# Kernel optimization log

Hardware: AMD Instinct MI355X
Metric: run time of the kernel (lower is better)

## Reference

```python
import jax, jax.numpy as jnp
import numpy as np

N, C, C_OUT, E = 50000, 128, 256, 600000


def setup_inputs() -> dict:
    key = jax.random.key(0)
    k1, k2, k3, k4, k5 = jax.random.split(key, 5)
    x = jax.random.normal(k1, (N, C), dtype=jnp.float32)
    edge_index = jax.random.randint(k2, (2, E), 0, N, dtype=jnp.int64)
    # torch Linear(2C -> C_OUT): weight [out, in], bias [out]
    bound = 1.0 / np.sqrt(2 * C)
    W = jax.random.uniform(k3, (C_OUT, 2 * C), dtype=jnp.float32, minval=-bound, maxval=bound)
    b = jax.random.uniform(k4, (C_OUT,), dtype=jnp.float32, minval=-bound, maxval=bound)
    return {"x": x, "edge_index": edge_index, "W": W, "b": b}


def reference(x, edge_index, W, b):
    src, dst = edge_index[0], edge_index[1]
    # gather - subtract: relative features per edge [E, C]
    rel = x[src] - x[dst]
    # scatter-max into destination nodes; empty segments -> 0 (torch_scatter fill)
    x_j = jax.ops.segment_max(rel, dst, num_segments=N)
    x_j = jnp.where(jnp.isfinite(x_j), x_j, 0.0)
    # concat + Linear + ReLU (MLP([2C, C_OUT], act='relu'))
    h = jnp.concatenate([x, x_j], axis=1)  # [N, 2C]
    out = h @ W.T + b
    return jax.nn.relu(out)
```

## Files before the change

### kernel.cpp

```cpp
#include <hip/hip_runtime.h>

#define NNODES 50000
#define CIN    128
#define COUT   256
#define KTOT   256

#define POISON 0xAAAAAAAAu

typedef float  f32x4  __attribute__((ext_vector_type(4)));
typedef short  bf16x8 __attribute__((ext_vector_type(8)));

#define GLOAD16(gptr, lptr) __builtin_amdgcn_global_load_lds(                      \
    (const __attribute__((address_space(1))) void*)(gptr),                         \
    (__attribute__((address_space(3))) void*)(lptr), 16, 0, 0)

__device__ __forceinline__ unsigned short f2bf(float f) {
    union { float f; unsigned int u; } v; v.f = f;
    unsigned int r = v.u + 0x7FFFu + ((v.u >> 16) & 1u);
    return (unsigned short)(r >> 16);
}
__device__ __forceinline__ float bf2f(unsigned short u) {
    return __uint_as_float((unsigned int)u << 16);
}

#define PX 1600000
#define PW (PX + 16384)

__global__ __launch_bounds__(256)
void prep_hist(const float* __restrict__ x, const float* __restrict__ W,
               const int* __restrict__ dst,
               unsigned short* __restrict__ xcat, unsigned short* __restrict__ Wbf,
               int* __restrict__ cnt, int E) {
    int g = blockIdx.x * 256 + threadIdx.x;
    if (g < PX) {
        float4 v = ((const float4*)x)[g];
        int row = g >> 5;
        int col = (g & 31) * 4;
        *(ushort4*)(xcat + (size_t)row * KTOT + col) =
            make_ushort4(f2bf(v.x), f2bf(v.y), f2bf(v.z), f2bf(v.w));
    } else if (g < PW) {
        int i = g - PX;
        float4 v = ((const float4*)W)[i];
        *(ushort4*)(Wbf + (size_t)i * 4) =
            make_ushort4(f2bf(v.x), f2bf(v.y), f2bf(v.z), f2bf(v.w));
    } else {
        int i = g - PW;
        if (i < E) atomicAdd(&cnt[dst[i]], 1);
    }
}

__global__ __launch_bounds__(256)
void scan_kernel(const int* __restrict__ cnt, int* __restrict__ row_start) {
    __shared__ int red[256];
    __shared__ int s[256];
    const int tid    = threadIdx.x;
    const int chunk0 = blockIdx.x * 256;

    int acc = 0;
    for (int i = tid; i < chunk0; i += 256)
        acc += (int)((unsigned)cnt[i] - POISON);
    red[tid] = acc;
    __syncthreads();
    for (int off = 128; off > 0; off >>= 1) {
        if (tid < off) red[tid] += red[tid + off];
        __syncthreads();
    }
    int base = red[0];

    int i = chunk0 + tid;
    int v = (i < NNODES) ? (int)((unsigned)cnt[i] - POISON) : 0;
    s[tid] = v;
    __syncthreads();
    for (int off = 1; off < 256; off <<= 1) {
        int t = (tid >= off) ? s[tid - off] : 0;
        __syncthreads();
        s[tid] += t;
        __syncthreads();
    }
    if (i < NNODES) row_start[i] = base + s[tid] - v;
    if (i == NNODES - 1) row_start[NNODES] = base + s[tid];
}

__global__ void scatter_kernel(const int* __restrict__ src, const int* __restrict__ dst,
                               const int* __restrict__ row_start, int* __restrict__ cnt,
                               int* __restrict__ sorted_src, int E) {
    int i = blockIdx.x * blockDim.x + threadIdx.x;
    if (i < E) {
        int d = dst[i];
        int old = atomicSub(&cnt[d], 1);
        int pos = (int)((unsigned)old - POISON) - 1;
        sorted_src[row_start[d] + pos] = src[i];
    }
}

__device__ __forceinline__ float2 fmax2(float2 a, float2 b) {
    return make_float2(fmaxf(a.x, b.x), fmaxf(a.y, b.y));
}

__global__ __launch_bounds__(256)
void gather_max_kernel(const float* __restrict__ x,
                       const int* __restrict__ row_start,
                       const int* __restrict__ sorted_src,
                       unsigned short* __restrict__ xcat) {
    int wid  = (blockIdx.x * blockDim.x + threadIdx.x) >> 6;
    int lane = threadIdx.x & 63;
    if (wid >= NNODES) return;

    int start = row_start[wid];
    int end   = row_start[wid + 1];

    const float NI = __int_as_float(0xFF800000u);
    float2 mm[8];
#pragma unroll
    for (int j = 0; j < 8; ++j) mm[j] = make_float2(NI, NI);

    int t = start;
    for (; t + 8 <= end; t += 8) {
        int     si[8];
        ushort2 uu[8];
#pragma unroll
        for (int j = 0; j < 8; ++j) si[j] = sorted_src[t + j];
#pragma unroll
        for (int j = 0; j < 8; ++j)
            uu[j] = *(const ushort2*)(xcat + (size_t)si[j] * KTOT + lane * 2);
#pragma unroll
        for (int j = 0; j < 8; ++j)
            mm[j] = fmax2(mm[j], make_float2(bf2f(uu[j].x), bf2f(uu[j].y)));
    }
    for (; t < end; ++t) {
        int s = sorted_src[t];
        ushort2 u = *(const ushort2*)(xcat + (size_t)s * KTOT + lane * 2);
        mm[0] = fmax2(mm[0], make_float2(bf2f(u.x), bf2f(u.y)));
    }
    float2 mx = fmax2(fmax2(fmax2(mm[0], mm[1]), fmax2(mm[2], mm[3])),
                      fmax2(fmax2(mm[4], mm[5]), fmax2(mm[6], mm[7])));

    float2 xv = ((const float2*)(x + (size_t)wid * CIN))[lane];
    bool nonempty = (end > start);
    float2 o;
    o.x = nonempty ? mx.x - xv.x : 0.0f;
    o.y = nonempty ? mx.y - xv.y : 0.0f;
    *((ushort2*)(xcat + (size_t)wid * KTOT + CIN + lane * 2)) =
        make_ushort2(f2bf(o.x), f2bf(o.y));
}

__global__ __launch_bounds__(256, 4)
void mfma_gemm(const unsigned short* __restrict__ xcat,
               const unsigned short* __restrict__ Wbf,
               const float* __restrict__ bias,
               float* __restrict__ out) {
    __shared__ unsigned short As[2][64][32];
    __shared__ unsigned short Bs[2][256][32];

    const int M = NNODES;
    const int m0 = blockIdx.x * 64;

    const int tid  = threadIdx.x;
    const int lane = tid & 63;
    const int wid  = tid >> 6;

    f32x4 acc[4][4] = {};

    auto stage = [&](int b, int kt) {
        {
            int row  = tid >> 2;
            int kseg = (tid & 3) * 8;
            int ks   = kseg ^ ((row & 3) << 3);
            int grow = m0 + row; if (grow > M - 1) grow = M - 1;
            GLOAD16(xcat + (size_t)grow * KTOT + kt + ks, &As[b][row][kseg]);
        }
#pragma unroll
        for (int j = 0; j < 4; ++j) {
            int u    = j * 256 + tid;
            int row  = u >> 2;
            int kseg = (u & 3) * 8;
            int ks   = kseg ^ ((row & 3) << 3);
            GLOAD16(Wbf + (size_t)row * KTOT + kt + ks, &Bs[b][row][kseg]);
        }
    };

    stage(0, 0);
    __syncthreads();

    const int l15 = lane & 15;
    const int kh  = (lane >> 4) * 8;
    const int khs = kh ^ ((l15 & 3) << 3);

#pragma unroll
    for (int t = 0; t < 8; ++t) {
        int b = t & 1;
        if (t < 7) stage(b ^ 1, (t + 1) * 32);

        bf16x8 af[4], bfr[4];
#pragma unroll
        for (int m = 0; m < 4; ++m)
            af[m] = *(const bf16x8*)&As[b][m * 16 + l15][khs];
#pragma unroll
        for (int n = 0; n < 4; ++n)
            bfr[n] = *(const bf16x8*)&Bs[b][wid * 64 + n * 16 + l15][khs];
#pragma unroll
        for (int m = 0; m < 4; ++m)
#pragma unroll
            for (int n = 0; n < 4; ++n)
                acc[m][n] = __builtin_amdgcn_mfma_f32_16x16x32_bf16(af[m], bfr[n], acc[m][n], 0, 0, 0);

        __syncthreads();
    }

#pragma unroll
    for (int n = 0; n < 4; ++n) {
        int col = wid * 64 + n * 16 + l15;
        float bv = bias[col];
#pragma unroll
        for (int m = 0; m < 4; ++m) {
            int r0 = m0 + m * 16 + ((lane >> 4) << 2);
            f32x4 a = acc[m][n];
#pragma unroll
            for (int r = 0; r < 4; ++r) {
                int rr = r0 + r;
                if (rr < M) out[(size_t)rr * COUT + col] = fmaxf(a[r] + bv, 0.0f);
            }
        }
    }
}

extern "C" void kernel_launch(void* const* d_in, const int* in_sizes, int n_in,
                              void* d_out, int out_size, void* d_ws, size_t ws_size,
                              hipStream_t stream) {
    const float* x  = (const float*)d_in[0];
    const int*   ei = (const int*)d_in[1];
    const float* W  = (const float*)d_in[2];
    const float* b  = (const float*)d_in[3];
    float*       out = (float*)d_out;

    const int E = in_sizes[1] / 2;
    const int* src = ei;
    const int* dst = ei + E;

    unsigned short* xcat       = (unsigned short*)d_ws;
    unsigned short* Wbf        = xcat + (size_t)NNODES * KTOT;
    int*            cnt        = (int*)(Wbf + COUT * KTOT);
    int*            row_start  = cnt + NNODES;
    int*            sorted_src = row_start + (NNODES + 1);

    const int NB_N = (NNODES + 255) / 256;
    const int NB_E = (E + 255) / 256;

    prep_hist<<<(PW + E + 255) / 256, 256, 0, stream>>>(x, W, dst, xcat, Wbf, cnt, E);
    scan_kernel<<<NB_N, 256, 0, stream>>>(cnt, row_start);
    scatter_kernel<<<NB_E, 256, 0, stream>>>(src, dst, row_start, cnt, sorted_src, E);
    gather_max_kernel<<<(NNODES * 64 + 255) / 256, 256, 0, stream>>>(x, row_start, sorted_src, xcat);
    mfma_gemm<<<(NNODES + 63) / 64, 256, 0, stream>>>(xcat, Wbf, b, out);
}
```

Measured before the change: 228.4 us.

## Fuse gather-max aggregation into the GEMM kernel via shared memory

Merges the per-node gather-max kernel into the MFMA GEMM. Each block computes the x_j half of its 64-row A tile directly into LDS, with swizzled columns, while the x half and the first W tile are loaded asynchronously. This removes one kernel launch and the global write and re-read of the x_j half of xcat. In exchange the GEMM block holds more LDS and runs at lower occupancy, and the irregular gather now runs with fewer waves, one node at a time per wave, before the MFMA loop starts.

```diff
diff --git a/kernel.cpp b/kernel.cpp
--- a/kernel.cpp
+++ b/kernel.cpp
@@ -97,78 +97,25 @@
     return make_float2(fmaxf(a.x, b.x), fmaxf(a.y, b.y));
 }
 
-__global__ __launch_bounds__(256)
-void gather_max_kernel(const float* __restrict__ x,
-                       const int* __restrict__ row_start,
-                       const int* __restrict__ sorted_src,
-                       unsigned short* __restrict__ xcat) {
-    int wid  = (blockIdx.x * blockDim.x + threadIdx.x) >> 6;
-    int lane = threadIdx.x & 63;
-    if (wid >= NNODES) return;
-
-    int start = row_start[wid];
-    int end   = row_start[wid + 1];
-
-    const float NI = __int_as_float(0xFF800000u);
-    float2 mm[8];
-#pragma unroll
-    for (int j = 0; j < 8; ++j) mm[j] = make_float2(NI, NI);
-
-    int t = start;
-    for (; t + 8 <= end; t += 8) {
-        int     si[8];
-        ushort2 uu[8];
-#pragma unroll
-        for (int j = 0; j < 8; ++j) si[j] = sorted_src[t + j];
-#pragma unroll
-        for (int j = 0; j < 8; ++j)
-            uu[j] = *(const ushort2*)(xcat + (size_t)si[j] * KTOT + lane * 2);
-#pragma unroll
-        for (int j = 0; j < 8; ++j)
-            mm[j] = fmax2(mm[j], make_float2(bf2f(uu[j].x), bf2f(uu[j].y)));
-    }
-    for (; t < end; ++t) {
-        int s = sorted_src[t];
-        ushort2 u = *(const ushort2*)(xcat + (size_t)s * KTOT + lane * 2);
-        mm[0] = fmax2(mm[0], make_float2(bf2f(u.x), bf2f(u.y)));
-    }
-    float2 mx = fmax2(fmax2(fmax2(mm[0], mm[1]), fmax2(mm[2], mm[3])),
-                      fmax2(fmax2(mm[4], mm[5]), fmax2(mm[6], mm[7])));
-
-    float2 xv = ((const float2*)(x + (size_t)wid * CIN))[lane];
-    bool nonempty = (end > start);
-    float2 o;
-    o.x = nonempty ? mx.x - xv.x : 0.0f;
-    o.y = nonempty ? mx.y - xv.y : 0.0f;
-    *((ushort2*)(xcat + (size_t)wid * KTOT + CIN + lane * 2)) =
-        make_ushort2(f2bf(o.x), f2bf(o.y));
-}
-
-__global__ __launch_bounds__(256, 4)
-void mfma_gemm(const unsigned short* __restrict__ xcat,
-               const unsigned short* __restrict__ Wbf,
-               const float* __restrict__ bias,
-               float* __restrict__ out) {
-    __shared__ unsigned short As[2][64][32];
+__global__ __launch_bounds__(256, 2)
+void mrconv_gemm(const float* __restrict__ x,
+                 const unsigned short* __restrict__ xcat,
+                 const unsigned short* __restrict__ Wbf,
+                 const int* __restrict__ row_start,
+                 const int* __restrict__ sorted_src,
+                 const float* __restrict__ bias,
+                 float* __restrict__ out) {
+    __shared__ unsigned short As [64][128];
+    __shared__ unsigned short Axj[64][128];
     __shared__ unsigned short Bs[2][256][32];
 
-    const int M = NNODES;
-    const int m0 = blockIdx.x * 64;
-
+    const int M    = NNODES;
+    const int m0   = blockIdx.x * 64;
     const int tid  = threadIdx.x;
     const int lane = tid & 63;
-    const int wid  = tid >> 6;
-
-    f32x4 acc[4][4] = {};
-
-    auto stage = [&](int b, int kt) {
-        {
-            int row  = tid >> 2;
-            int kseg = (tid & 3) * 8;
-            int ks   = kseg ^ ((row & 3) << 3);
-            int grow = m0 + row; if (grow > M - 1) grow = M - 1;
-            GLOAD16(xcat + (size_t)grow * KTOT + kt + ks, &As[b][row][kseg]);
-        }
+    const int wv   = tid >> 6;
+
+    auto stageB = [&](int b, int kt) {
 #pragma unroll
         for (int j = 0; j < 4; ++j) {
             int u    = j * 256 + tid;
@@ -179,25 +126,82 @@
         }
     };
 
-    stage(0, 0);
+#pragma unroll
+    for (int j = 0; j < 4; ++j) {
+        int u   = j * 256 + tid;
+        int row = u >> 4;
+        int g   = u & 15;
+        int gs  = (g & 8) | ((g & 7) ^ (row & 7));
+        int grow = m0 + row; if (grow > M - 1) grow = M - 1;
+        GLOAD16(xcat + (size_t)grow * KTOT + gs * 8, &As[row][g * 8]);
+    }
+    stageB(0, 0);
+
+    const float NI = __int_as_float(0xFF800000u);
+    for (int i = 0; i < 16; ++i) {
+        int r    = wv * 16 + i;
+        int node = m0 + r; if (node > M - 1) node = M - 1;
+        int start = row_start[node];
+        int end   = row_start[node + 1];
+
+        float2 mm[8];
+#pragma unroll
+        for (int j = 0; j < 8; ++j) mm[j] = make_float2(NI, NI);
+
+        int t = start;
+        for (; t + 8 <= end; t += 8) {
+            int     si[8];
+            ushort2 uu[8];
+#pragma unroll
+            for (int j = 0; j < 8; ++j) si[j] = sorted_src[t + j];
+#pragma unroll
+            for (int j = 0; j < 8; ++j)
+                uu[j] = *(const ushort2*)(xcat + (size_t)si[j] * KTOT + lane * 2);
+#pragma unroll
+            for (int j = 0; j < 8; ++j)
+                mm[j] = fmax2(mm[j], make_float2(bf2f(uu[j].x), bf2f(uu[j].y)));
+        }
+        for (; t < end; ++t) {
+            int s = sorted_src[t];
+            ushort2 u = *(const ushort2*)(xcat + (size_t)s * KTOT + lane * 2);
+            mm[0] = fmax2(mm[0], make_float2(bf2f(u.x), bf2f(u.y)));
+        }
+        float2 mx = fmax2(fmax2(fmax2(mm[0], mm[1]), fmax2(mm[2], mm[3])),
+                          fmax2(fmax2(mm[4], mm[5]), fmax2(mm[6], mm[7])));
+
+        float2 xv = ((const float2*)(x + (size_t)node * CIN))[lane];
+        bool nonempty = (end > start);
+        float2 o;
+        o.x = nonempty ? mx.x - xv.x : 0.0f;
+        o.y = nonempty ? mx.y - xv.y : 0.0f;
+        int c = (lane * 2) ^ ((i & 7) << 3);
+        *(ushort2*)&Axj[r][c] = make_ushort2(f2bf(o.x), f2bf(o.y));
+    }
+
     __syncthreads();
 
     const int l15 = lane & 15;
     const int kh  = (lane >> 4) * 8;
-    const int khs = kh ^ ((l15 & 3) << 3);
+    const int l7s = (l15 & 7) << 3;
+    const int khsB = kh ^ ((l15 & 3) << 3);
+
+    f32x4 acc[4][4] = {};
 
 #pragma unroll
     for (int t = 0; t < 8; ++t) {
         int b = t & 1;
-        if (t < 7) stage(b ^ 1, (t + 1) * 32);
+        if (t < 7) stageB(b ^ 1, (t + 1) * 32);
 
         bf16x8 af[4], bfr[4];
 #pragma unroll
-        for (int m = 0; m < 4; ++m)
-            af[m] = *(const bf16x8*)&As[b][m * 16 + l15][khs];
+        for (int m = 0; m < 4; ++m) {
+            int row = m * 16 + l15;
+            if (t < 4) af[m] = *(const bf16x8*)&As [row][(t * 32 + kh) ^ l7s];
+            else       af[m] = *(const bf16x8*)&Axj[row][((t - 4) * 32 + kh) ^ l7s];
+        }
 #pragma unroll
         for (int n = 0; n < 4; ++n)
-            bfr[n] = *(const bf16x8*)&Bs[b][wid * 64 + n * 16 + l15][khs];
+            bfr[n] = *(const bf16x8*)&Bs[b][wv * 64 + n * 16 + l15][khsB];
 #pragma unroll
         for (int m = 0; m < 4; ++m)
 #pragma unroll
@@ -209,7 +213,7 @@
 
 #pragma unroll
     for (int n = 0; n < 4; ++n) {
-        int col = wid * 64 + n * 16 + l15;
+        int col = wv * 64 + n * 16 + l15;
         float bv = bias[col];
 #pragma unroll
         for (int m = 0; m < 4; ++m) {
@@ -249,6 +253,5 @@
     prep_hist<<<(PW + E + 255) / 256, 256, 0, stream>>>(x, W, dst, xcat, Wbf, cnt, E);
     scan_kernel<<<NB_N, 256, 0, stream>>>(cnt, row_start);
     scatter_kernel<<<NB_E, 256, 0, stream>>>(src, dst, row_start, cnt, sorted_src, E);
-    gather_max_kernel<<<(NNODES * 64 + 255) / 256, 256, 0, stream>>>(x, row_start, sorted_src, xcat);
-    mfma_gemm<<<(NNODES + 63) / 64, 256, 0, stream>>>(xcat, Wbf, b, out);
-}
+    mrconv_gemm<<<(NNODES + 63) / 64, 256, 0, stream>>>(x, xcat, Wbf, row_start, sorted_src, b, out);
+}
```

Result: slower. 306.1 us (+34.0%).
